# Performance work log

Hardware: AMD Instinct MI355X
Metric: run time of the kernel (lower is better)

Reference implementation:

```python
import jax, jax.numpy as jnp
import numpy as np

T, B, D, H = 512, 256, 256, 256


def setup_inputs() -> dict:
    key = jax.random.key(0)
    ks = jax.random.split(key, 8)
    x = jax.random.normal(ks[0], (T, B, D), dtype=jnp.float32)
    h0 = jax.random.normal(ks[1], (1, B, H), dtype=jnp.float32)
    c0 = jax.random.normal(ks[2], (1, B, H), dtype=jnp.float32)
    W_ih = jax.random.normal(ks[3], (4 * H, D), dtype=jnp.float32) / np.sqrt(D)
    W_hh = jax.random.normal(ks[4], (4 * H, H), dtype=jnp.float32) / np.sqrt(H)
    b_ih = jnp.zeros((4 * H,), dtype=jnp.float32)
    b_hh = jnp.zeros((4 * H,), dtype=jnp.float32)
    done = jax.random.randint(ks[5], (T, B), 0, 2, dtype=jnp.int32)
    return {"x": x, "h0": h0, "c0": c0, "W_ih": W_ih, "W_hh": W_hh,
            "b_ih": b_ih, "b_hh": b_hh, "done": done}


def reference(x, h0, c0, W_ih, W_hh, b_ih, b_hh, done):
    done_f = done.astype(x.dtype)  # [T, B]
    # Precompute input contribution to gates for all timesteps: [T, B, 4H]
    gx = jnp.einsum('tbd,gd->tbg', x, W_ih) + b_ih + b_hh

    def step(carry, inp):
        h, c = carry                      # [B, H] each
        gxt, dt = inp                     # [B, 4H], [B]
        mask = (1.0 - dt)[:, None]        # reset hidden state where done
        h = h * mask
        c = c * mask
        gates = gxt + jnp.einsum('bh,gh->bg', h, W_hh)  # [B, 4H]
        i, f, g, o = jnp.split(gates, 4, axis=-1)       # PyTorch LSTM gate order
        c = jax.nn.sigmoid(f) * c + jax.nn.sigmoid(i) * jnp.tanh(g)
        h = jax.nn.sigmoid(o) * jnp.tanh(c)
        return (h, c), h

    (hT, cT), feats = jax.lax.scan(step, (h0[0], c0[0]), (gx, done_f))
    rnn_feature = feats.reshape(T * B, H)
    return rnn_feature, hT[None], cT[None]
```

## Files before the change

kernel.cpp:

```cpp
#include <hip/hip_runtime.h>
#include <math.h>

#define T_DIM 512
#define B_DIM 256
#define D_DIM 256
#define H_DIM 256
#define G_DIM 1024
#define K_DIM 512
#define NROUNDS 40
#define CHAIN_K 16
#define AB_ROW 1024

typedef __attribute__((ext_vector_type(8))) short short8;
typedef __attribute__((ext_vector_type(4))) float f32x4;

__device__ __forceinline__ unsigned int f2bf(float f) {
    unsigned int b = __float_as_uint(f);
    return (b + 0x7FFFu + ((b >> 16) & 1u)) >> 16;
}
__device__ __forceinline__ float bf2f(unsigned short us) {
    return __uint_as_float((unsigned int)us << 16);
}
__device__ __forceinline__ unsigned long long pack4(float4 v) {
    const unsigned int lo = (f2bf(v.y) << 16) | f2bf(v.x);
    const unsigned int hi = (f2bf(v.w) << 16) | f2bf(v.z);
    return ((unsigned long long)hi << 32) | lo;
}
__device__ __forceinline__ float sigm(float x) { return 1.0f / (1.0f + __expf(-x)); }
__device__ __forceinline__ float tanh_fast(float x) { return 2.0f / (1.0f + __expf(-2.0f * x)) - 1.0f; }

__device__ __forceinline__ void dma16(const void* g, void* l) {
    __builtin_amdgcn_global_load_lds(
        (const __attribute__((address_space(1))) void*)g,
        (__attribute__((address_space(3))) void*)l, 16, 0, 0);
}

__global__ __launch_bounds__(256) void k_prep_weights(
    const float* __restrict__ W_ih, const float* __restrict__ W_hh,
    const float* __restrict__ b_ih, const float* __restrict__ b_hh,
    unsigned int* __restrict__ Wb, float* __restrict__ bias)
{
    const int idx = blockIdx.x * 256 + threadIdx.x;
    const int jp = idx & 3, l = (idx >> 2) & 63, ks = (idx >> 8) & 15, nt = idx >> 12;
    const int g = nt * 16 + (l & 15);
    const int k0 = ks * 32 + ((l >> 4) << 3) + 2 * jp;
    const float w0 = (k0 < D_DIM) ? W_ih[g * D_DIM + k0] : W_hh[g * H_DIM + (k0 - D_DIM)];
    const float w1 = (k0 + 1 < D_DIM) ? W_ih[g * D_DIM + k0 + 1] : W_hh[g * H_DIM + (k0 + 1 - D_DIM)];
    Wb[idx] = (f2bf(w1) << 16) | f2bf(w0);
    if (idx < G_DIM) bias[idx] = b_ih[idx] + b_hh[idx];
}

__global__ __launch_bounds__(256) void k_prep_wq(
    const float* __restrict__ W_ih, const float* __restrict__ W_hh,
    unsigned long long* __restrict__ Wq)
{
    const int idx = blockIdx.x * 256 + threadIdx.x;
    const int kq = idx >> 10, g = idx & (G_DIM - 1);
    float w[4];
    #pragma unroll
    for (int j = 0; j < 4; ++j) {
        const int k = kq * 4 + j;
        w[j] = (k < D_DIM) ? W_ih[g * D_DIM + k] : W_hh[g * H_DIM + (k - D_DIM)];
    }
    Wq[idx] = pack4((float4){w[0], w[1], w[2], w[3]});
}

__global__ __launch_bounds__(256) void k_prep_ab(
    const float* __restrict__ x, const float* __restrict__ h0,
    const int* __restrict__ done, unsigned long long* __restrict__ ab_u64)
{
    const int wv = (blockIdx.x * 256 + threadIdx.x) >> 6;
    const int l = threadIdx.x & 63;
    const int pos = wv;
    const float4 xv = *(const float4*)(x + (size_t)pos * D_DIM + l * 4);
    ab_u64[(size_t)pos * (AB_ROW / 4) + l] = pack4(xv);
    const int d = done[pos];
    if (d || pos < B_DIM) {
        unsigned long long hv = 0ull;
        if (!d) {
            const float4 h = *(const float4*)(h0 + (size_t)(pos & (B_DIM - 1)) * H_DIM + l * 4);
            hv = pack4(h);
        }
        ab_u64[(size_t)pos * (AB_ROW / 4) + 64 + l] = hv;
    }
}

__global__ __launch_bounds__(256) void k_kmap(
    const int* __restrict__ done, int* __restrict__ kmap, int* __restrict__ counts)
{
    __shared__ int lcnt[NROUNDS];
    const int tid = threadIdx.x;
    if (tid < NROUNDS) lcnt[tid] = 0;
    __syncthreads();
    const int t = blockIdx.x, b = tid;
    int kv = t;
    for (int tt = t; tt >= 0; --tt) {
        if (done[tt * B_DIM + b]) { kv = t - tt; break; }
    }
    kmap[t * B_DIM + b] = kv;
    const int bin = kv < NROUNDS ? kv : NROUNDS - 1;
    atomicAdd(&lcnt[bin], 1);
    __syncthreads();
    if (tid < NROUNDS && lcnt[tid] > 0) atomicAdd(&counts[tid], lcnt[tid]);
}

__global__ __launch_bounds__(64) void k_offs(
    const int* __restrict__ counts, int* __restrict__ offs, int* __restrict__ cursor)
{
    if (threadIdx.x == 0) {
        int s = 0;
        for (int i = 0; i < NROUNDS; ++i) { offs[i] = s; s += counts[i]; }
    }
    if (threadIdx.x < NROUNDS) cursor[threadIdx.x] = 0;
}

__global__ __launch_bounds__(256) void k_scatter(
    const int* __restrict__ kmap, const int* __restrict__ offs,
    int* __restrict__ cursor, int* __restrict__ rowlist)
{
    __shared__ int lcnt[NROUNDS];
    __shared__ int gbase[NROUNDS];
    const int tid = threadIdx.x;
    if (tid < NROUNDS) lcnt[tid] = 0;
    __syncthreads();
    const int pos = blockIdx.x * 256 + tid;
    const int kv0 = kmap[pos];
    const int kv = kv0 < NROUNDS ? kv0 : NROUNDS - 1;
    const int lrank = atomicAdd(&lcnt[kv], 1);
    __syncthreads();
    if (tid < NROUNDS && lcnt[tid] > 0) gbase[tid] = atomicAdd(&cursor[tid], lcnt[tid]);
    __syncthreads();
    rowlist[offs[kv] + gbase[kv] + lrank] = pos;
}

__global__ __launch_bounds__(512, 1) void k_round(
    const short* __restrict__ ab, const float* __restrict__ c0,
    const int* __restrict__ done,
    const short* __restrict__ Wb, const float* __restrict__ bias,
    const int* __restrict__ counts, const int* __restrict__ offs,
    const int* __restrict__ rowlist,
    float* __restrict__ out,
    short* __restrict__ ab_w, int kk)
{
    __shared__ short A_lds[2 * 32 * 512];
    __shared__ float scr[4 * 64 * 36];
    const int nk = counts[kk];
    const int base = offs[kk];
    const int ntiles = (nk + 31) >> 5;

    int cb, rt, rstride;
    if ((gridDim.x & 255) == 0) {
        const int m = gridDim.x >> 8;
        const int xcd = blockIdx.x & 7, slot = blockIdx.x >> 3;
        cb = slot & 3;
        rt = xcd * (8 * m) + (slot >> 2);
        rstride = 64 * m;
    } else {
        cb = blockIdx.x & 3;
        rt = blockIdx.x >> 2;
        rstride = gridDim.x >> 2;
    }
    if (rt >= ntiles) return;

    const int tid = threadIdx.x;
    const int w = tid >> 6, l = tid & 63;
    const int lr = l >> 4, lc = l & 15;
    const int q = w & 3, gth = w >> 2;

    const int u_ep = cb * 64 + l;
    const float bI = bias[u_ep], bF = bias[256 + u_ep], bG = bias[512 + u_ep], bO = bias[768 + u_ep];
    const unsigned short* ab_us = (const unsigned short*)ab;

#define ISSUE_A(PP, bufv)                                                        \
    {                                                                            \
        _Pragma("unroll") for (int rr = 0; rr < 4; ++rr) {                       \
            const int r_ = w * 4 + rr;                                           \
            dma16(ab + (size_t)PP[rr] * AB_ROW + ((l ^ (r_ & 15)) << 3),         \
                  &A_lds[(bufv) * 16384 + r_ * 512]);                            \
        }                                                                        \
    }
#define LOAD_NEXT(row0v, PP, CP, DSm)                                            \
    {                                                                            \
        _Pragma("unroll") for (int j_ = 0; j_ < 4; ++j_) {                       \
            const int gr_ = (row0v) + w * 4 + j_;                                \
            PP[j_] = rowlist[base + (gr_ < nk ? gr_ : nk - 1)];                  \
        }                                                                        \
        DSm = 0;                                                                 \
        _Pragma("unroll") for (int j_ = 0; j_ < 4; ++j_) {                       \
            const int p_ = PP[j_];                                               \
            if (kk > 0) {                                                        \
                CP[j_] = bf2f(ab_us[(size_t)(p_ - B_DIM) * AB_ROW + 512 + u_ep]); \
            } else {                                                             \
                CP[j_] = done[p_] ? 0.0f : c0[(size_t)(p_ & (B_DIM - 1)) * H_DIM + u_ep]; \
            }                                                                    \
            const int sp_ = p_ + B_DIM;                                          \
            const int d_ = (sp_ < T_DIM * B_DIM) ? done[sp_] : 1;                \
            DSm |= d_ << j_;                                                     \
        }                                                                        \
    }

    int posC[4]; float cpC[4]; int dsmC;
    LOAD_NEXT(rt * 32, posC, cpC, dsmC);
    ISSUE_A(posC, 0);
    short8 breg0[16], breg1[16];
    {
        const int nt0 = (2 * gth + 0) * 16 + cb * 4 + q;
        const int nt1 = (2 * gth + 1) * 16 + cb * 4 + q;
        #pragma unroll
        for (int ks = 0; ks < 16; ++ks) {
            breg0[ks] = *(const short8*)(Wb + (((size_t)nt0 * 16 + ks) * 64 + l) * 8);
            breg1[ks] = *(const short8*)(Wb + (((size_t)nt1 * 16 + ks) * 64 + l) * 8);
        }
        #pragma unroll
        for (int ks = 0; ks < 16; ++ks) {
            asm volatile("" : "+v"(breg0[ks]));
            asm volatile("" : "+v"(breg1[ks]));
        }
    }

    int buf = 0;
    for (; rt < ntiles; rt += rstride) {
        const int row0 = rt * 32;

        asm volatile("s_waitcnt vmcnt(0) lgkmcnt(0)" ::: "memory");
        __builtin_amdgcn_sched_barrier(0);
        __builtin_amdgcn_s_barrier();
        __builtin_amdgcn_sched_barrier(0);
        const int rtn = rt + rstride;
        const bool more = (rtn < ntiles);
        int posN[4]; float cpN[4]; int dsmN = 0;
        if (more) {
            LOAD_NEXT(rtn * 32, posN, cpN, dsmN);
            ISSUE_A(posN, buf ^ 1);
        }

        f32x4 acc0[2], acc1[2];
        #pragma unroll
        for (int mb = 0; mb < 2; ++mb) { acc0[mb] = (f32x4){0,0,0,0}; acc1[mb] = (f32x4){0,0,0,0}; }
        #pragma unroll
        for (int ks = 0; ks < 16; ++ks) {
            #pragma unroll
            for (int mb = 0; mb < 2; ++mb) {
                const short8 a = *(const short8*)&A_lds[buf * 16384 + (mb * 16 + lc) * 512
                                                       + (((ks * 4 + lr) ^ lc) << 3)];
                acc0[mb] = __builtin_amdgcn_mfma_f32_16x16x32_bf16(a, breg0[ks], acc0[mb], 0, 0, 0);
                acc1[mb] = __builtin_amdgcn_mfma_f32_16x16x32_bf16(a, breg1[ks], acc1[mb], 0, 0, 0);
            }
        }

        #pragma unroll
        for (int mb = 0; mb < 2; ++mb) {
            *(f32x4*)&scr[(((2 * gth + 0) * 64 + q * 16 + lc) * 36) + mb * 16 + lr * 4] = acc0[mb];
            *(f32x4*)&scr[(((2 * gth + 1) * 64 + q * 16 + lc) * 36) + mb * 16 + lr * 4] = acc1[mb];
        }
        asm volatile("s_waitcnt lgkmcnt(0)" ::: "memory");
        __builtin_amdgcn_sched_barrier(0);
        __builtin_amdgcn_s_barrier();
        __builtin_amdgcn_sched_barrier(0);

        const f32x4 vi = *(const f32x4*)&scr[((0 * 64 + l) * 36) + w * 4];
        const f32x4 vf = *(const f32x4*)&scr[((1 * 64 + l) * 36) + w * 4];
        const f32x4 vg = *(const f32x4*)&scr[((2 * 64 + l) * 36) + w * 4];
        const f32x4 vo = *(const f32x4*)&scr[((3 * 64 + l) * 36) + w * 4];
        #pragma unroll
        for (int j = 0; j < 4; ++j) {
            const int gr = row0 + w * 4 + j;
            if (gr < nk) {
                const int pos = posC[j];
                const float cp = cpC[j];
                const float si = sigm(vi[j] + bI);
                const float sf = sigm(vf[j] + bF);
                const float tg = tanh_fast(vg[j] + bG);
                const float so = sigm(vo[j] + bO);
                const float cn = sf * cp + si * tg;
                const float hn = so * tanh_fast(cn);
                out[(size_t)pos * H_DIM + u_ep] = hn;
                ab_w[(size_t)pos * AB_ROW + 512 + u_ep] = (short)f2bf(cn);
                if (kk + 1 < CHAIN_K && !((dsmC >> j) & 1))
                    ab_w[(size_t)(pos + B_DIM) * AB_ROW + 256 + u_ep] = (short)f2bf(hn);
            }
        }

        #pragma unroll
        for (int j = 0; j < 4; ++j) { posC[j] = posN[j]; cpC[j] = cpN[j]; }
        dsmC = dsmN;
        buf ^= 1;
    }
#undef ISSUE_A
#undef LOAD_NEXT
}

__global__ __launch_bounds__(1024) void k_finish(
    const float* __restrict__ x, const unsigned long long* __restrict__ Wq,
    const float* __restrict__ bias,
    const int* __restrict__ counts, const int* __restrict__ offs,
    const int* __restrict__ rowlist, const int* __restrict__ kmap,
    float* __restrict__ out, short* __restrict__ ab)
{
    __shared__ float abuf[K_DIM];
    __shared__ float dots[G_DIM];
    const int g = threadIdx.x;
    const int nch = counts[CHAIN_K];
    const unsigned short* ab_us = (const unsigned short*)ab;

    for (int m = blockIdx.x; m < nch; m += gridDim.x) {
        const int pos0 = rowlist[offs[CHAIN_K] + m];
        float c_u = 0.0f;
        if (g < H_DIM) {
            abuf[H_DIM + g] = out[(size_t)(pos0 - B_DIM) * H_DIM + g];
            c_u = bf2f(ab_us[(size_t)(pos0 - B_DIM) * AB_ROW + 512 + g]);
        }
        int pos = pos0, step = CHAIN_K;
        while (true) {
            if (g < H_DIM) abuf[g] = x[(size_t)pos * D_DIM + g];
            __syncthreads();
            float dot = bias[g];
            #pragma unroll 8
            for (int kq = 0; kq < K_DIM / 4; ++kq) {
                const unsigned long long wq = Wq[(size_t)kq * G_DIM + g];
                const float4 a = *(const float4*)&abuf[kq * 4];
                const unsigned int wlo = (unsigned int)wq;
                const unsigned int whi = (unsigned int)(wq >> 32);
                const float w0 = __uint_as_float(wlo << 16);
                const float w1 = __uint_as_float(wlo & 0xFFFF0000u);
                const float w2 = __uint_as_float(whi << 16);
                const float w3 = __uint_as_float(whi & 0xFFFF0000u);
                dot = fmaf(a.x, w0, dot);
                dot = fmaf(a.y, w1, dot);
                dot = fmaf(a.z, w2, dot);
                dot = fmaf(a.w, w3, dot);
            }
            dots[g] = dot;
            __syncthreads();
            if (g < H_DIM) {
                const float si = sigm(dots[g]);
                const float sf = sigm(dots[H_DIM + g]);
                const float tg = tanh_fast(dots[2 * H_DIM + g]);
                const float so = sigm(dots[3 * H_DIM + g]);
                c_u = sf * c_u + si * tg;
                const float hn = so * tanh_fast(c_u);
                out[(size_t)pos * H_DIM + g] = hn;
                ab[(size_t)pos * AB_ROW + 512 + g] = (short)f2bf(c_u);
                abuf[H_DIM + g] = hn;
            }
            pos += B_DIM;
            ++step;
            __syncthreads();
            if (pos >= T_DIM * B_DIM) break;
            if (kmap[pos] != step) break;
        }
        __syncthreads();
    }
}

__global__ __launch_bounds__(256) void k_final(const short* __restrict__ ab, float* __restrict__ out)
{
    const size_t i = (size_t)blockIdx.x * 256 + threadIdx.x;
    const size_t featN = (size_t)T_DIM * B_DIM * H_DIM;
    const size_t last  = (size_t)(T_DIM - 1) * B_DIM * H_DIM;
    out[featN + i] = out[last + i];
    const int b = (int)(i >> 8), u = (int)(i & 255);
    const size_t pos = (size_t)(T_DIM - 1) * B_DIM + b;
    out[featN + (size_t)B_DIM * H_DIM + i] =
        bf2f(((const unsigned short*)ab)[pos * AB_ROW + 512 + u]);
}

__global__ __launch_bounds__(64) void k_zero(int* __restrict__ counts)
{
    if (threadIdx.x < NROUNDS) counts[threadIdx.x] = 0;
}

extern "C" void kernel_launch(void* const* d_in, const int* in_sizes, int n_in,
                              void* d_out, int out_size, void* d_ws, size_t ws_size,
                              hipStream_t stream)
{
    const float* x    = (const float*)d_in[0];
    const float* h0   = (const float*)d_in[1];
    const float* c0   = (const float*)d_in[2];
    const float* W_ih = (const float*)d_in[3];
    const float* W_hh = (const float*)d_in[4];
    const float* b_ih = (const float*)d_in[5];
    const float* b_hh = (const float*)d_in[6];
    const int*   done = (const int*)d_in[7];
    float* out = (float*)d_out;

    const size_t TB = (size_t)T_DIM * B_DIM;
    char* ws = (char*)d_ws;
    size_t off = 0;
    unsigned int* Wb = (unsigned int*)(ws + off); off += (size_t)(K_DIM / 2) * G_DIM * 4;
    unsigned long long* Wq = (unsigned long long*)(ws + off); off += (size_t)(K_DIM / 4) * G_DIM * 8;
    float* bias = (float*)(ws + off);             off += (size_t)G_DIM * 4;
    int* kmap    = (int*)(ws + off);              off += TB * 4;
    int* rowlist = (int*)(ws + off);              off += TB * 4;
    int* counts  = (int*)(ws + off);              off += 256;
    int* offs    = (int*)(ws + off);              off += 256;
    int* cursor  = (int*)(ws + off);              off += 256;
    off = (off + 255) & ~(size_t)255;
    short* ab = (short*)(ws + off);               off += TB * AB_ROW * 2;

    k_zero<<<1, 64, 0, stream>>>(counts);
    k_prep_weights<<<1024, 256, 0, stream>>>(W_ih, W_hh, b_ih, b_hh, Wb, bias);
    k_prep_wq<<<512, 256, 0, stream>>>(W_ih, W_hh, Wq);
    k_prep_ab<<<(int)(TB / 4), 256, 0, stream>>>(x, h0, done, (unsigned long long*)ab);
    k_kmap<<<T_DIM, 256, 0, stream>>>(done, kmap, counts);
    k_offs<<<1, 64, 0, stream>>>(counts, offs, cursor);
    k_scatter<<<(int)(TB / 256), 256, 0, stream>>>(kmap, offs, cursor, rowlist);

    int est = 70000;
    for (int k = 0; k < CHAIN_K; ++k) {
        int grid;
        if (est >= 8192)      grid = 512;
        else if (est >= 1024) grid = 256;
        else {
            int rgs = (est + 31) / 32;
            if (rgs < 1) rgs = 1;
            grid = 4 * rgs;
        }
        k_round<<<grid, 512, 0, stream>>>((const short*)ab, c0, done, (const short*)Wb,
                                          bias, counts, offs, rowlist, out, ab, k);
        est >>= 1;
    }
    k_finish<<<64, 1024, 0, stream>>>(x, Wq, bias, counts, offs, rowlist, kmap, out, ab);
    k_final<<<B_DIM * H_DIM / 256, 256, 0, stream>>>((const short*)ab, out);
}
```

Before: 627.0 us.

## Cap round grid at 256 blocks and relax per-tile waitcnt for prefetch overlap

Grid sizing for each chain round is unified to 4 blocks per row-group, capped at 256, so the 512-block variant and its generalized XCD mapping are dropped. The full vmcnt(0) barrier is moved before the loop and replaced inside the loop with a vmcnt(12) wait, so outstanding loads can stay in flight across tiles. The masked next-step h store becomes unconditional: it writes zero when done, and a redirected slot at the last timestep. This is meant to cut launch and sync overhead and branch divergence, but the partial waitcnt relies on exact instruction-count assumptions about which loads must have finished.

Measured after the change: 606.8 us. -3.2%, faster.

```diff
diff --git a/kernel.cpp b/kernel.cpp
--- a/kernel.cpp
+++ b/kernel.cpp
@@ -149,12 +149,11 @@
     const int ntiles = (nk + 31) >> 5;
 
     int cb, rt, rstride;
-    if ((gridDim.x & 255) == 0) {
-        const int m = gridDim.x >> 8;
+    if (gridDim.x == 256) {
         const int xcd = blockIdx.x & 7, slot = blockIdx.x >> 3;
         cb = slot & 3;
-        rt = xcd * (8 * m) + (slot >> 2);
-        rstride = 64 * m;
+        rt = xcd * 8 + (slot >> 2);
+        rstride = 64;
     } else {
         cb = blockIdx.x & 3;
         rt = blockIdx.x >> 2;
@@ -211,21 +210,25 @@
             breg0[ks] = *(const short8*)(Wb + (((size_t)nt0 * 16 + ks) * 64 + l) * 8);
             breg1[ks] = *(const short8*)(Wb + (((size_t)nt1 * 16 + ks) * 64 + l) * 8);
         }
-        #pragma unroll
-        for (int ks = 0; ks < 16; ++ks) {
-            asm volatile("" : "+v"(breg0[ks]));
-            asm volatile("" : "+v"(breg1[ks]));
-        }
-    }
+    }
+    asm volatile("s_waitcnt vmcnt(0) lgkmcnt(0)" ::: "memory");
+    __builtin_amdgcn_sched_barrier(0);
+    __builtin_amdgcn_s_barrier();
+    __builtin_amdgcn_sched_barrier(0);
 
     int buf = 0;
+    bool first = true;
     for (; rt < ntiles; rt += rstride) {
         const int row0 = rt * 32;
 
-        asm volatile("s_waitcnt vmcnt(0) lgkmcnt(0)" ::: "memory");
-        __builtin_amdgcn_sched_barrier(0);
-        __builtin_amdgcn_s_barrier();
-        __builtin_amdgcn_sched_barrier(0);
+        if (!first) {
+            asm volatile("s_waitcnt vmcnt(12) lgkmcnt(0)" ::: "memory");
+            __builtin_amdgcn_sched_barrier(0);
+            __builtin_amdgcn_s_barrier();
+            __builtin_amdgcn_sched_barrier(0);
+        }
+        first = false;
+
         const int rtn = rt + rstride;
         const bool more = (rtn < ntiles);
         int posN[4]; float cpN[4]; int dsmN = 0;
@@ -276,8 +279,9 @@
                 const float hn = so * tanh_fast(cn);
                 out[(size_t)pos * H_DIM + u_ep] = hn;
                 ab_w[(size_t)pos * AB_ROW + 512 + u_ep] = (short)f2bf(cn);
-                if (kk + 1 < CHAIN_K && !((dsmC >> j) & 1))
-                    ab_w[(size_t)(pos + B_DIM) * AB_ROW + 256 + u_ep] = (short)f2bf(hn);
+                const short hv = ((dsmC >> j) & 1) ? (short)0 : (short)f2bf(hn);
+                ab_w[(size_t)(pos + B_DIM < T_DIM * B_DIM ? pos + B_DIM : pos) * AB_ROW
+                     + (pos + B_DIM < T_DIM * B_DIM ? 256 + u_ep : 768 + u_ep)] = hv;
             }
         }
 
@@ -408,16 +412,11 @@
 
     int est = 70000;
     for (int k = 0; k < CHAIN_K; ++k) {
-        int grid;
-        if (est >= 8192)      grid = 512;
-        else if (est >= 1024) grid = 256;
-        else {
-            int rgs = (est + 31) / 32;
-            if (rgs < 1) rgs = 1;
-            grid = 4 * rgs;
-        }
-        k_round<<<grid, 512, 0, stream>>>((const short*)ab, c0, done, (const short*)Wb,
-                                          bias, counts, offs, rowlist, out, ab, k);
+        int rgs = (est + 31) / 32;
+        if (rgs > 64) rgs = 64;
+        if (rgs < 1) rgs = 1;
+        k_round<<<4 * rgs, 512, 0, stream>>>((const short*)ab, c0, done, (const short*)Wb,
+                                             bias, counts, offs, rowlist, out, ab, k);
         est >>= 1;
     }
     k_finish<<<64, 1024, 0, stream>>>(x, Wq, bias, counts, offs, rowlist, kmap, out, ab);
```
